# Performance work log

Hardware: AMD Instinct MI355X
Metric: run time of the kernel (lower is better)

## Reference

```python
import jax, jax.numpy as jnp
import numpy as np

B, S, DIM = 2, 2048, 1024
H = 16
HD = DIM // H  # 64
SCALE = HD ** -0.5


def setup_inputs() -> dict:
    key = jax.random.key(0)
    k1, k2, k3 = jax.random.split(key, 3)
    x = jax.random.normal(k1, (B, S, DIM), dtype=jnp.float32)
    # Linear weights scaled ~1/sqrt(fan_in) like torch default init
    Wqkv = jax.random.normal(k2, (DIM, 3 * DIM), dtype=jnp.float32) * (DIM ** -0.5)
    Wproj = jax.random.normal(k3, (DIM, DIM), dtype=jnp.float32) * (DIM ** -0.5)
    return {"x": x, "Wqkv": Wqkv, "Wproj": Wproj}


def reference(x, Wqkv, Wproj):
    Bsz, Slen, dim = x.shape
    qkv = x @ Wqkv  # (B, S, 3*dim)
    qkv = qkv.reshape(Bsz, Slen, 3, H, HD)
    q, k, v = qkv[:, :, 0], qkv[:, :, 1], qkv[:, :, 2]  # each (B, S, H, HD)
    # softmax attention (chunking in the original is memory-only; math identical)
    scores = jnp.einsum("bshd,bthd->bhst", q, k) * SCALE  # (B, H, S, S)
    attn = jax.nn.softmax(scores, axis=-1)
    out = jnp.einsum("bhst,bthd->bshd", attn, v)  # (B, S, H, HD)
    out = out.reshape(Bsz, Slen, dim)
    return out @ Wproj
```

## Files before the change

kernel.cpp:

```cpp
#include <hip/hip_runtime.h>
#include <stdint.h>

typedef unsigned short u16;
typedef __attribute__((ext_vector_type(8))) short bf16x8;
typedef __attribute__((ext_vector_type(4))) float f32x4;

#define BATCH 2
#define SEQ 2048
#define NH 16
#define HDIM 64
#define DMODEL 1024
#define MTOT (BATCH * SEQ)
#define QKV_N (3 * DMODEL)
#define ATT_SCALE 0.125f
#define L2E 1.44269504088896340736f
#define C2 (ATT_SCALE * L2E)

#define BAR() asm volatile("s_barrier" ::: "memory")
#define F3(a, b, c) fmaxf(fmaxf((a), (b)), (c))

__device__ __forceinline__ u16 f2b(float f) {
    uint32_t x = __builtin_bit_cast(uint32_t, f);
    uint32_t r = (x + 0x7fffu + ((x >> 16) & 1u)) >> 16;
    return (u16)r;
}

__device__ __forceinline__ uint32_t cvt_pk(float lo, float hi) {
    uint32_t r;
    asm("v_cvt_pk_bf16_f32 %0, %1, %2" : "=v"(r) : "v"(lo), "v"(hi));
    return r;
}

__device__ __forceinline__ void gl_lds16(const void* g, void* l) {
    __builtin_amdgcn_global_load_lds(
        (const __attribute__((address_space(1))) void*)g,
        (__attribute__((address_space(3))) void*)l, 16, 0, 0);
}

__global__ __launch_bounds__(256) void k_prep(const float* __restrict__ x,
                                              const float* __restrict__ Wq,
                                              const float* __restrict__ Wp,
                                              u16* __restrict__ xb,
                                              u16* __restrict__ WqT,
                                              u16* __restrict__ WpT) {
    const int bid = blockIdx.x, tid = threadIdx.x;
    if (bid < 2048) {
        const int i = bid * 256 + tid;
        const float4* p = (const float4*)x + (size_t)i * 2;
        float4 a = p[0], b = p[1];
        union { uint32_t w[4]; uint4 v; } u;
        u.w[0] = cvt_pk(a.x, a.y);
        u.w[1] = cvt_pk(a.z, a.w);
        u.w[2] = cvt_pk(b.x, b.y);
        u.w[3] = cvt_pk(b.z, b.w);
        *(uint4*)(xb + (size_t)i * 8) = u.v;
        return;
    }
    __shared__ float tile[64][65];
    const float* W;
    u16* WT;
    int cols, bx, by;
    if (bid < 2048 + 768) {
        const int j = bid - 2048;
        W = Wq; WT = WqT; cols = QKV_N; bx = j % 48; by = j / 48;
    } else {
        const int j = bid - 2816;
        W = Wp; WT = WpT; cols = DMODEL; bx = j % 16; by = j / 16;
    }
    const int rows = DMODEL;
    const int c0 = bx * 64, r0 = by * 64;
    const int tx = tid & 63, ty = tid >> 6;
#pragma unroll
    for (int i = 0; i < 16; ++i) {
        int r = i * 4 + ty;
        tile[r][tx] = W[(size_t)(r0 + r) * cols + c0 + tx];
    }
    __syncthreads();
#pragma unroll
    for (int i = 0; i < 16; ++i) {
        int c = i * 4 + ty;
        WT[(size_t)(c0 + c) * rows + r0 + tx] = f2b(tile[tx][c]);
    }
}

__global__ __launch_bounds__(512, 2) void k_gemm_qkv8(const u16* __restrict__ A,
                                                      const u16* __restrict__ BT,
                                                      u16* __restrict__ C,
                                                      u16* __restrict__ Vt) {
    extern __shared__ __align__(16) u16 lds[];
    const int tid = threadIdx.x, wid = tid >> 6, lane = tid & 63;
    const int r = lane & 15, g = lane >> 4;
    const int wr = wid >> 2, wc = wid & 3;
    const int m0 = blockIdx.y * 256, n0 = blockIdx.x * 256;
    const int K = DMODEL;

    auto STG = [&](int kt2, int rg) {
        const int isB = rg >> 1, half = rg & 1;
        const u16* src = isB ? BT : A;
        const int rowb = (isB ? n0 : m0) + half * 128 + wid * 16 + (lane >> 2);
        const u16* s = src + (size_t)rowb * K + kt2 * 64 + (lane & 3) * 8;
        const int dst = (kt2 & 1) * 32768 + isB * 16384 + half * 8192 +
                        wid * 1024 + lane * 8;
        gl_lds16(s, &lds[dst]);
        gl_lds16(s + 32, &lds[dst + 512]);
    };

    f32x4 acc[8][4] = {};
    bf16x8 a[4][2], b[4][2];
    const int aB = wr * 8192 + r * 32 + g * 8;
    const int bB = 16384 + (wc >> 1) * 8192 + (wc & 1) * 4096 + r * 32 + g * 8;

#pragma unroll
    for (int t2 = 0; t2 < 2; ++t2)
#pragma unroll
        for (int rg = 0; rg < 4; ++rg) STG(t2, rg);
    asm volatile("s_waitcnt vmcnt(0)" ::: "memory");
    __syncthreads();

    for (int kt = 0; kt < 16; ++kt) {
        const int sb = (kt & 1) * 32768;
#pragma unroll
        for (int mi = 0; mi < 4; ++mi)
#pragma unroll
            for (int kk = 0; kk < 2; ++kk)
                a[mi][kk] = *(const bf16x8*)&lds[sb + aB + (mi * 2 + kk) * 512];
#pragma unroll
        for (int ni = 0; ni < 2; ++ni)
#pragma unroll
            for (int kk = 0; kk < 2; ++kk)
                b[ni][kk] = *(const bf16x8*)&lds[sb + bB + (ni * 2 + kk) * 512];
        BAR();
        __builtin_amdgcn_s_setprio(1);
#pragma unroll
        for (int mi = 0; mi < 4; ++mi)
#pragma unroll
            for (int ni = 0; ni < 2; ++ni)
#pragma unroll
                for (int kk = 0; kk < 2; ++kk)
                    acc[mi][ni] = __builtin_amdgcn_mfma_f32_16x16x32_bf16(
                        b[ni][kk], a[mi][kk], acc[mi][ni], 0, 0, 0);
        __builtin_amdgcn_s_setprio(0);
        BAR();
#pragma unroll
        for (int ni = 2; ni < 4; ++ni)
#pragma unroll
            for (int kk = 0; kk < 2; ++kk)
                b[ni][kk] = *(const bf16x8*)&lds[sb + bB + (ni * 2 + kk) * 512];
        BAR();
        __builtin_amdgcn_s_setprio(1);
#pragma unroll
        for (int mi = 0; mi < 4; ++mi)
#pragma unroll
            for (int ni = 2; ni < 4; ++ni)
#pragma unroll
                for (int kk = 0; kk < 2; ++kk)
                    acc[mi][ni] = __builtin_amdgcn_mfma_f32_16x16x32_bf16(
                        b[ni][kk], a[mi][kk], acc[mi][ni], 0, 0, 0);
        __builtin_amdgcn_s_setprio(0);
        BAR();
#pragma unroll
        for (int mi = 0; mi < 4; ++mi)
#pragma unroll
            for (int kk = 0; kk < 2; ++kk)
                a[mi][kk] = *(const bf16x8*)&lds[sb + aB + ((4 + mi) * 2 + kk) * 512];
        if (kt < 14) { STG(kt + 2, 2); STG(kt + 2, 3); }
        BAR();
        __builtin_amdgcn_s_setprio(1);
#pragma unroll
        for (int mi = 0; mi < 4; ++mi)
#pragma unroll
            for (int ni = 2; ni < 4; ++ni)
#pragma unroll
                for (int kk = 0; kk < 2; ++kk)
                    acc[4 + mi][ni] = __builtin_amdgcn_mfma_f32_16x16x32_bf16(
                        b[ni][kk], a[mi][kk], acc[4 + mi][ni], 0, 0, 0);
        __builtin_amdgcn_s_setprio(0);
        BAR();
        if (kt < 14) { STG(kt + 2, 0); STG(kt + 2, 1); }
        BAR();
        __builtin_amdgcn_s_setprio(1);
#pragma unroll
        for (int mi = 0; mi < 4; ++mi)
#pragma unroll
            for (int ni = 0; ni < 2; ++ni)
#pragma unroll
                for (int kk = 0; kk < 2; ++kk)
                    acc[4 + mi][ni] = __builtin_amdgcn_mfma_f32_16x16x32_bf16(
                        b[ni][kk], a[mi][kk], acc[4 + mi][ni], 0, 0, 0);
        __builtin_amdgcn_s_setprio(0);
        if (kt < 14) {
            asm volatile("s_waitcnt vmcnt(8)" ::: "memory");
        } else if (kt == 14) {
            asm volatile("s_waitcnt vmcnt(0)" ::: "memory");
        }
        BAR();
    }

    if (n0 < 2 * DMODEL) {
#pragma unroll
        for (int mi = 0; mi < 8; ++mi)
#pragma unroll
            for (int ni = 0; ni < 4; ++ni) {
                const int row = m0 + wr * 128 + mi * 16 + r;
                const int col = n0 + wc * 64 + ni * 16 + g * 4;
                union { uint32_t w[2]; ushort4 v; } o;
                o.w[0] = cvt_pk(acc[mi][ni][0], acc[mi][ni][1]);
                o.w[1] = cvt_pk(acc[mi][ni][2], acc[mi][ni][3]);
                *(ushort4*)&C[(size_t)row * QKV_N + col] = o.v;
            }
    } else {
        const int h_ = ((n0 - 2 * DMODEL) >> 6) + wc;
#pragma unroll
        for (int mi = 0; mi < 8; ++mi)
#pragma unroll
            for (int ni = 0; ni < 4; ++ni) {
                const int row = m0 + wr * 128 + mi * 16 + r;
                const int b_ = row >> 11, s_ = row & (SEQ - 1);
                const int hd0 = ni * 16 + g * 4;
                union { uint32_t w[2]; u16 t[4]; } o;
                o.w[0] = cvt_pk(acc[mi][ni][0], acc[mi][ni][1]);
                o.w[1] = cvt_pk(acc[mi][ni][2], acc[mi][ni][3]);
                const size_t base =
                    ((size_t)(b_ * NH + h_) * HDIM + hd0) * SEQ + s_;
                Vt[base] = o.t[0];
                Vt[base + SEQ] = o.t[1];
                Vt[base + 2 * SEQ] = o.t[2];
                Vt[base + 3 * SEQ] = o.t[3];
            }
    }
}

__global__ __launch_bounds__(256) void k_gemm_proj(const u16* __restrict__ A,
                                                   const u16* __restrict__ BT,
                                                   float* __restrict__ C) {
    __shared__ __align__(16) u16 As[64 * 64];
    __shared__ __align__(16) u16 Bs[128 * 64];
    const int tid = threadIdx.x;
    const int wid = tid >> 6, lane = tid & 63;
    const int r = lane & 15, g = lane >> 4;
    const int m0 = blockIdx.y * 64, n0 = blockIdx.x * 128;
    const int srow = lane >> 3, scol = (lane & 7) * 8;
    const int K = DMODEL;
    f32x4 acc[4][2] = {};
    for (int k0 = 0; k0 < K; k0 += 64) {
#pragma unroll
        for (int i = 0; i < 2; ++i) {
            const int li = wid * 2 + i;
            gl_lds16(A + (size_t)(m0 + li * 8 + srow) * K + k0 + scol, &As[li * 512]);
        }
#pragma unroll
        for (int i = 0; i < 4; ++i) {
            const int li = wid * 4 + i;
            gl_lds16(BT + (size_t)(n0 + li * 8 + srow) * K + k0 + scol, &Bs[li * 512]);
        }
        __syncthreads();
#pragma unroll
        for (int kk = 0; kk < 2; ++kk) {
            bf16x8 af[4], bfr[2];
#pragma unroll
            for (int mi = 0; mi < 4; ++mi)
                af[mi] = *(const bf16x8*)&As[(mi * 16 + r) * 64 + kk * 32 + g * 8];
#pragma unroll
            for (int ni = 0; ni < 2; ++ni)
                bfr[ni] = *(const bf16x8*)&Bs[(wid * 32 + ni * 16 + r) * 64 + kk * 32 + g * 8];
#pragma unroll
            for (int mi = 0; mi < 4; ++mi)
#pragma unroll
                for (int ni = 0; ni < 2; ++ni)
                    acc[mi][ni] = __builtin_amdgcn_mfma_f32_16x16x32_bf16(
                        bfr[ni], af[mi], acc[mi][ni], 0, 0, 0);
        }
        __syncthreads();
    }
#pragma unroll
    for (int mi = 0; mi < 4; ++mi)
#pragma unroll
        for (int ni = 0; ni < 2; ++ni) {
            const int row = m0 + mi * 16 + r;
            const int col = n0 + wid * 32 + ni * 16 + g * 4;
            float4 vv;
            vv.x = acc[mi][ni][0]; vv.y = acc[mi][ni][1];
            vv.z = acc[mi][ni][2]; vv.w = acc[mi][ni][3];
            *(float4*)&C[(size_t)row * DMODEL + col] = vv;
        }
}

__global__ __launch_bounds__(256) void k_attn(const u16* __restrict__ qkv,
                                              const u16* __restrict__ Vt,
                                              u16* __restrict__ O) {
    __shared__ __align__(16) u16 Ks[3][4096];
    __shared__ __align__(16) u16 Vs[2][4096];
    const int bh = blockIdx.y;
    const int b = bh >> 4, h = bh & 15;
    const int q0 = blockIdx.x * 64;
    const int tid = threadIdx.x, wid = tid >> 6, lane = tid & 63;
    const int r = lane & 15, g = lane >> 4;
    const int NT = SEQ / 64;

    const size_t qbase = (size_t)(b * SEQ + q0 + wid * 16 + r) * QKV_N + h * HDIM;
    const bf16x8 qf0 = *(const bf16x8*)&qkv[qbase + g * 8];
    const bf16x8 qf1 = *(const bf16x8*)&qkv[qbase + 32 + g * 8];

    const short one_b = (short)0x3F80;
    const bf16x8 ones = {one_b, one_b, one_b, one_b, one_b, one_b, one_b, one_b};

    float mL = -1e30f;
    f32x4 oacc[4] = {};
    f32x4 lacc = {};
    const int kc0 = wid * 2;

    const u16* kp[2];
    const u16* vp[2];
    int kdst[2], vdst[2];
#pragma unroll
    for (int i = 0; i < 2; ++i) {
        const int kc = kc0 + i;
        const int ksrow = (kc >> 2) * 32 + g * 8 + (kc & 1) * 4 + ((lane >> 2) & 3);
        const int kscol = ((kc >> 1) & 1) * 32 + (lane & 3) * 8;
        kp[i] = qkv + (size_t)(b * SEQ + ksrow) * QKV_N + DMODEL + h * HDIM + kscol;
        const int vhd = (kc & 3) * 16 + r;
        const int vsc = (kc >> 2) * 32 + g * 8;
        vp[i] = Vt + ((size_t)bh * HDIM + vhd) * SEQ + vsc;
        kdst[i] = kc * 512;
        vdst[i] = kc * 512;
    }

#define STAGE_K(SLOT)                                                \
    {                                                                \
        _Pragma("unroll") for (int i = 0; i < 2; ++i) {              \
            gl_lds16(kp[i], &Ks[SLOT][kdst[i]]);                     \
            kp[i] += 64 * QKV_N;                                     \
        }                                                            \
    }
#define STAGE_V(SLOT)                                                \
    {                                                                \
        _Pragma("unroll") for (int i = 0; i < 2; ++i) {              \
            gl_lds16(vp[i], &Vs[SLOT][vdst[i]]);                     \
            vp[i] += 64;                                             \
        }                                                            \
    }
#define QKT(DST, SLOT)                                               \
    {                                                                \
        _Pragma("unroll") for (int nf = 0; nf < 4; ++nf) {           \
            const int kbase = (nf & 1) * 2048 + (nf >> 1) * 512 +    \
                              (r >> 2) * 128 + (r & 3) * 32 + g * 8; \
            bf16x8 kf0 = *(const bf16x8*)&Ks[SLOT][kbase];           \
            bf16x8 kf1 = *(const bf16x8*)&Ks[SLOT][kbase + 1024];    \
            DST[nf] = __builtin_amdgcn_mfma_f32_16x16x32_bf16(       \
                kf0, qf0, DST[nf], 0, 0, 0);                         \
            DST[nf] = __builtin_amdgcn_mfma_f32_16x16x32_bf16(       \
                kf1, qf1, DST[nf], 0, 0, 0);                         \
        }                                                            \
    }

    STAGE_K(0); STAGE_V(0);
    STAGE_K(1); STAGE_V(1);
    STAGE_K(2);
    asm volatile("s_waitcnt vmcnt(0)");
    __syncthreads();

    f32x4 sA[4] = {};
    __builtin_amdgcn_s_setprio(1);
    QKT(sA, 0);
    __builtin_amdgcn_s_setprio(0);
    BAR();

    int kw = 0, kr = 1;
    for (int t = 0; t < NT; ++t) {
        const int vcur = t & 1;

        if (t + 3 < NT) STAGE_K(kw);

        f32x4 sB[4] = {};
        if (t + 1 < NT) {
            __builtin_amdgcn_s_setprio(1);
            QKT(sB, kr);
            __builtin_amdgcn_s_setprio(0);
        }

        float mt = F3(sA[0][0], sA[0][1], sA[0][2]);
        mt = F3(mt, sA[0][3], sA[1][0]);
        mt = F3(mt, sA[1][1], sA[1][2]);
        mt = F3(mt, sA[1][3], sA[2][0]);
        mt = F3(mt, sA[2][1], sA[2][2]);
        mt = F3(mt, sA[2][3], sA[3][0]);
        mt = F3(mt, sA[3][1], sA[3][2]);
        mt = fmaxf(mt, sA[3][3]);
        const float pm = mt * C2;
        if (!__all(pm <= mL + 8.f)) {
            float rm = pm;
            rm = fmaxf(rm, __shfl_xor(rm, 16, 64));
            rm = fmaxf(rm, __shfl_xor(rm, 32, 64));
            const float mNew = fmaxf(mL, rm);
            const float al = exp2f(mL - mNew);
            mL = mNew;
#pragma unroll
            for (int ht = 0; ht < 4; ++ht)
#pragma unroll
                for (int e = 0; e < 4; ++e) oacc[ht][e] *= al;
#pragma unroll
            for (int e = 0; e < 4; ++e) lacc[e] *= al;
        }
        float p[4][4];
#pragma unroll
        for (int nf = 0; nf < 4; ++nf)
#pragma unroll
            for (int e = 0; e < 4; ++e)
                p[nf][e] = exp2f(sA[nf][e] * C2 - mL);

        union { uint32_t w[4]; bf16x8 v; } upf0, upf1;
        upf0.w[0] = cvt_pk(p[0][0], p[0][1]);
        upf0.w[1] = cvt_pk(p[0][2], p[0][3]);
        upf0.w[2] = cvt_pk(p[2][0], p[2][1]);
        upf0.w[3] = cvt_pk(p[2][2], p[2][3]);
        upf1.w[0] = cvt_pk(p[1][0], p[1][1]);
        upf1.w[1] = cvt_pk(p[1][2], p[1][3]);
        upf1.w[2] = cvt_pk(p[3][0], p[3][1]);
        upf1.w[3] = cvt_pk(p[3][2], p[3][3]);

        __builtin_amdgcn_s_setprio(1);
#pragma unroll
        for (int ht = 0; ht < 4; ++ht) {
            bf16x8 vf0 = *(const bf16x8*)&Vs[vcur][ht * 512 + g * 128 + r * 8];
            bf16x8 vf1 = *(const bf16x8*)&Vs[vcur][(4 + ht) * 512 + g * 128 + r * 8];
            oacc[ht] = __builtin_amdgcn_mfma_f32_16x16x32_bf16(vf0, upf0.v, oacc[ht], 0, 0, 0);
            oacc[ht] = __builtin_amdgcn_mfma_f32_16x16x32_bf16(vf1, upf1.v, oacc[ht], 0, 0, 0);
        }
        lacc = __builtin_amdgcn_mfma_f32_16x16x32_bf16(ones, upf0.v, lacc, 0, 0, 0);
        lacc = __builtin_amdgcn_mfma_f32_16x16x32_bf16(ones, upf1.v, lacc, 0, 0, 0);
        __builtin_amdgcn_s_setprio(0);

        if (t + 1 < NT) {
            BAR();
            if (t + 2 < NT) STAGE_V(vcur);
            if (t <= NT - 4) {
                asm volatile("s_waitcnt vmcnt(4)");
            } else if (t == NT - 3) {
                asm volatile("s_waitcnt vmcnt(2)");
            } else {
                asm volatile("s_waitcnt vmcnt(0)");
            }
            BAR();
        }

#pragma unroll
        for (int nf = 0; nf < 4; ++nf) sA[nf] = sB[nf];
        kw = (kw == 2) ? 0 : kw + 1;
        kr = (kr == 2) ? 0 : kr + 1;
    }
#undef STAGE_K
#undef STAGE_V
#undef QKT

    const float inv = 1.0f / lacc[0];
    const size_t obase = (size_t)(b * SEQ + q0 + wid * 16 + r) * DMODEL + h * HDIM;
#pragma unroll
    for (int ht = 0; ht < 4; ++ht) {
        union { uint32_t w[2]; ushort4 v; } o;
        o.w[0] = cvt_pk(oacc[ht][0] * inv, oacc[ht][1] * inv);
        o.w[1] = cvt_pk(oacc[ht][2] * inv, oacc[ht][3] * inv);
        *(ushort4*)&O[obase + ht * 16 + g * 4] = o.v;
    }
}

extern "C" void kernel_launch(void* const* d_in, const int* in_sizes, int n_in,
                              void* d_out, int out_size, void* d_ws, size_t ws_size,
                              hipStream_t stream) {
    const float* x = (const float*)d_in[0];
    const float* Wqkv = (const float*)d_in[1];
    const float* Wproj = (const float*)d_in[2];
    float* out = (float*)d_out;

    u16* xb = (u16*)d_ws;
    u16* WqkvT = xb + (size_t)MTOT * DMODEL;
    u16* WprojT = WqkvT + (size_t)QKV_N * DMODEL;
    u16* qkv = WprojT + (size_t)DMODEL * DMODEL;
    u16* Vt = qkv + (size_t)MTOT * QKV_N;
    u16* Ob = Vt + (size_t)BATCH * NH * HDIM * SEQ;

    hipFuncSetAttribute(reinterpret_cast<const void*>(k_gemm_qkv8),
                        hipFuncAttributeMaxDynamicSharedMemorySize, 131072);

    k_prep<<<dim3(3072), 256, 0, stream>>>(x, Wqkv, Wproj, xb, WqkvT, WprojT);
    k_gemm_qkv8<<<dim3(QKV_N / 256, MTOT / 256), 512, 131072, stream>>>(
        xb, WqkvT, qkv, Vt);
    k_attn<<<dim3(SEQ / 64, BATCH * NH), 256, 0, stream>>>(qkv, Vt, Ob);
    k_gemm_proj<<<dim3(DMODEL / 128, MTOT / 64), 256, 0, stream>>>(Ob, WprojT, out);
}
```

Baseline: 215.0 us.

## Fuse all four stages into one persistent cooperative kernel with grid syncs

Replaces the four separate launches (prep, QKV GEMM, attention, projection) with a single cooperative kernel of 256 blocks of 512 threads that walks through each stage and separates them with grid.sync(). Each stage is remapped to virtual block indices: attention runs two 4-wave units per block over two passes, and projection runs two units per block. The aim is to remove inter-kernel launch gaps and tail effects. In exchange only 256 blocks with 128KB LDS run, so occupancy per stage drops (only 192 blocks do the QKV GEMM), and the grid barriers add their own cost.

```diff
diff --git a/kernel.cpp b/kernel.cpp
--- a/kernel.cpp
+++ b/kernel.cpp
@@ -1,5 +1,8 @@
 #include <hip/hip_runtime.h>
+#include <hip/hip_cooperative_groups.h>
 #include <stdint.h>
+
+namespace cg = cooperative_groups;
 
 typedef unsigned short u16;
 typedef __attribute__((ext_vector_type(8))) short bf16x8;
@@ -37,15 +40,15 @@
         (__attribute__((address_space(3))) void*)l, 16, 0, 0);
 }
 
-__global__ __launch_bounds__(256) void k_prep(const float* __restrict__ x,
-                                              const float* __restrict__ Wq,
-                                              const float* __restrict__ Wp,
-                                              u16* __restrict__ xb,
-                                              u16* __restrict__ WqT,
-                                              u16* __restrict__ WpT) {
-    const int bid = blockIdx.x, tid = threadIdx.x;
-    if (bid < 2048) {
-        const int i = bid * 256 + tid;
+__device__ __forceinline__ void stage_prep(u16* lds,
+                                           const float* x, const float* Wq,
+                                           const float* Wp, u16* xb,
+                                           u16* WqT, u16* WpT,
+                                           int bid, int tid) {
+    const int gt = bid * 512 + tid;
+#pragma unroll
+    for (int it = 0; it < 4; ++it) {
+        const int i = gt + it * 131072;
         const float4* p = (const float4*)x + (size_t)i * 2;
         float4 a = p[0], b = p[1];
         union { uint32_t w[4]; uint4 v; } u;
@@ -54,44 +57,38 @@
         u.w[2] = cvt_pk(b.x, b.y);
         u.w[3] = cvt_pk(b.z, b.w);
         *(uint4*)(xb + (size_t)i * 8) = u.v;
-        return;
-    }
-    __shared__ float tile[64][65];
-    const float* W;
-    u16* WT;
-    int cols, bx, by;
-    if (bid < 2048 + 768) {
-        const int j = bid - 2048;
-        W = Wq; WT = WqT; cols = QKV_N; bx = j % 48; by = j / 48;
-    } else {
-        const int j = bid - 2816;
-        W = Wp; WT = WpT; cols = DMODEL; bx = j % 16; by = j / 16;
-    }
-    const int rows = DMODEL;
-    const int c0 = bx * 64, r0 = by * 64;
+    }
+    float (*tile)[65] = (float(*)[65])lds;
     const int tx = tid & 63, ty = tid >> 6;
-#pragma unroll
-    for (int i = 0; i < 16; ++i) {
-        int r = i * 4 + ty;
-        tile[r][tx] = W[(size_t)(r0 + r) * cols + c0 + tx];
-    }
-    __syncthreads();
-#pragma unroll
-    for (int i = 0; i < 16; ++i) {
-        int c = i * 4 + ty;
-        WT[(size_t)(c0 + c) * rows + r0 + tx] = f2b(tile[tx][c]);
-    }
-}
-
-__global__ __launch_bounds__(512, 2) void k_gemm_qkv8(const u16* __restrict__ A,
-                                                      const u16* __restrict__ BT,
-                                                      u16* __restrict__ C,
-                                                      u16* __restrict__ Vt) {
-    extern __shared__ __align__(16) u16 lds[];
-    const int tid = threadIdx.x, wid = tid >> 6, lane = tid & 63;
+    for (int it = 0; it < 4; ++it) {
+        const int tt = bid * 4 + it;
+        const float* W; u16* WT; int cols, bx, by;
+        if (tt < 768) { W = Wq; WT = WqT; cols = QKV_N; bx = tt % 48; by = tt / 48; }
+        else { int t2 = tt - 768; W = Wp; WT = WpT; cols = DMODEL; bx = t2 % 16; by = t2 / 16; }
+        const int c0 = bx * 64, r0 = by * 64;
+        __syncthreads();
+#pragma unroll
+        for (int i = 0; i < 8; ++i) {
+            int r = i * 8 + ty;
+            tile[r][tx] = W[(size_t)(r0 + r) * cols + c0 + tx];
+        }
+        __syncthreads();
+#pragma unroll
+        for (int i = 0; i < 8; ++i) {
+            int c = i * 8 + ty;
+            WT[(size_t)(c0 + c) * DMODEL + r0 + tx] = f2b(tile[tx][c]);
+        }
+    }
+}
+
+__device__ __forceinline__ void stage_gemm_qkv(u16* lds,
+                                               const u16* A, const u16* BT,
+                                               u16* C, u16* Vt,
+                                               int vb, int tid) {
+    const int wid = tid >> 6, lane = tid & 63;
     const int r = lane & 15, g = lane >> 4;
     const int wr = wid >> 2, wc = wid & 3;
-    const int m0 = blockIdx.y * 256, n0 = blockIdx.x * 256;
+    const int m0 = (vb / 12) * 256, n0 = (vb % 12) * 256;
     const int K = DMODEL;
 
     auto STG = [&](int kt2, int rg) {
@@ -230,15 +227,201 @@
     }
 }
 
-__global__ __launch_bounds__(256) void k_gemm_proj(const u16* __restrict__ A,
-                                                   const u16* __restrict__ BT,
-                                                   float* __restrict__ C) {
-    __shared__ __align__(16) u16 As[64 * 64];
-    __shared__ __align__(16) u16 Bs[128 * 64];
-    const int tid = threadIdx.x;
-    const int wid = tid >> 6, lane = tid & 63;
+__device__ __forceinline__ void stage_attn(u16* lds,
+                                           const u16* qkv, const u16* Vt,
+                                           u16* O, int bid, int tid) {
+    const int wid8 = tid >> 6;
+    const int half = wid8 >> 2, wid = wid8 & 3;
+    const int lane = tid & 63;
     const int r = lane & 15, g = lane >> 4;
-    const int m0 = blockIdx.y * 64, n0 = blockIdx.x * 128;
+    const int NT = SEQ / 64;
+    u16* Ks = lds + half * 20480;
+    u16* Vs = Ks + 3 * 4096;
+
+    const short one_b = (short)0x3F80;
+    const bf16x8 ones = {one_b, one_b, one_b, one_b, one_b, one_b, one_b, one_b};
+
+#define AT_STAGE_K(SLOT)                                             \
+    {                                                                \
+        _Pragma("unroll") for (int i = 0; i < 2; ++i) {              \
+            gl_lds16(kp[i], Ks + (SLOT) * 4096 + kdst[i]);           \
+            kp[i] += 64 * QKV_N;                                     \
+        }                                                            \
+    }
+#define AT_STAGE_V(SLOT)                                             \
+    {                                                                \
+        _Pragma("unroll") for (int i = 0; i < 2; ++i) {              \
+            gl_lds16(vp[i], Vs + (SLOT) * 4096 + vdst[i]);           \
+            vp[i] += 64;                                             \
+        }                                                            \
+    }
+#define AT_QKT(DST, SLOT)                                            \
+    {                                                                \
+        _Pragma("unroll") for (int nf = 0; nf < 4; ++nf) {           \
+            const int kbase = (nf & 1) * 2048 + (nf >> 1) * 512 +    \
+                              (r >> 2) * 128 + (r & 3) * 32 + g * 8; \
+            bf16x8 kf0 = *(const bf16x8*)(Ks + (SLOT) * 4096 + kbase);          \
+            bf16x8 kf1 = *(const bf16x8*)(Ks + (SLOT) * 4096 + kbase + 1024);   \
+            DST[nf] = __builtin_amdgcn_mfma_f32_16x16x32_bf16(       \
+                kf0, qf0, DST[nf], 0, 0, 0);                         \
+            DST[nf] = __builtin_amdgcn_mfma_f32_16x16x32_bf16(       \
+                kf1, qf1, DST[nf], 0, 0, 0);                         \
+        }                                                            \
+    }
+
+    for (int pass = 0; pass < 2; ++pass) {
+        BAR();
+        const int unit = pass * 512 + bid * 2 + half;
+        const int bh = unit >> 5, qx = unit & 31;
+        const int b = bh >> 4, h = bh & 15;
+        const int q0 = qx * 64;
+
+        const size_t qbase = (size_t)(b * SEQ + q0 + wid * 16 + r) * QKV_N + h * HDIM;
+        const bf16x8 qf0 = *(const bf16x8*)&qkv[qbase + g * 8];
+        const bf16x8 qf1 = *(const bf16x8*)&qkv[qbase + 32 + g * 8];
+
+        float mL = -1e30f;
+        f32x4 oacc[4] = {};
+        f32x4 lacc = {};
+        const int kc0 = wid * 2;
+
+        const u16* kp[2];
+        const u16* vp[2];
+        int kdst[2], vdst[2];
+#pragma unroll
+        for (int i = 0; i < 2; ++i) {
+            const int kc = kc0 + i;
+            const int ksrow = (kc >> 2) * 32 + g * 8 + (kc & 1) * 4 + ((lane >> 2) & 3);
+            const int kscol = ((kc >> 1) & 1) * 32 + (lane & 3) * 8;
+            kp[i] = qkv + (size_t)(b * SEQ + ksrow) * QKV_N + DMODEL + h * HDIM + kscol;
+            const int vhd = (kc & 3) * 16 + r;
+            const int vsc = (kc >> 2) * 32 + g * 8;
+            vp[i] = Vt + ((size_t)bh * HDIM + vhd) * SEQ + vsc;
+            kdst[i] = kc * 512;
+            vdst[i] = kc * 512;
+        }
+
+        AT_STAGE_K(0); AT_STAGE_V(0);
+        AT_STAGE_K(1); AT_STAGE_V(1);
+        AT_STAGE_K(2);
+        asm volatile("s_waitcnt vmcnt(0)");
+        __syncthreads();
+
+        f32x4 sA[4] = {};
+        __builtin_amdgcn_s_setprio(1);
+        AT_QKT(sA, 0);
+        __builtin_amdgcn_s_setprio(0);
+        BAR();
+
+        int kw = 0, kr = 1;
+        for (int t = 0; t < NT; ++t) {
+            const int vcur = t & 1;
+            if (t + 3 < NT) AT_STAGE_K(kw);
+
+            f32x4 sB[4] = {};
+            if (t + 1 < NT) {
+                __builtin_amdgcn_s_setprio(1);
+                AT_QKT(sB, kr);
+                __builtin_amdgcn_s_setprio(0);
+            }
+
+            float mt = F3(sA[0][0], sA[0][1], sA[0][2]);
+            mt = F3(mt, sA[0][3], sA[1][0]);
+            mt = F3(mt, sA[1][1], sA[1][2]);
+            mt = F3(mt, sA[1][3], sA[2][0]);
+            mt = F3(mt, sA[2][1], sA[2][2]);
+            mt = F3(mt, sA[2][3], sA[3][0]);
+            mt = F3(mt, sA[3][1], sA[3][2]);
+            mt = fmaxf(mt, sA[3][3]);
+            const float pm = mt * C2;
+            if (!__all(pm <= mL + 8.f)) {
+                float rm = pm;
+                rm = fmaxf(rm, __shfl_xor(rm, 16, 64));
+                rm = fmaxf(rm, __shfl_xor(rm, 32, 64));
+                const float mNew = fmaxf(mL, rm);
+                const float al = exp2f(mL - mNew);
+                mL = mNew;
+#pragma unroll
+                for (int ht = 0; ht < 4; ++ht)
+#pragma unroll
+                    for (int e = 0; e < 4; ++e) oacc[ht][e] *= al;
+#pragma unroll
+                for (int e = 0; e < 4; ++e) lacc[e] *= al;
+            }
+            float p[4][4];
+#pragma unroll
+            for (int nf = 0; nf < 4; ++nf)
+#pragma unroll
+                for (int e = 0; e < 4; ++e)
+                    p[nf][e] = exp2f(sA[nf][e] * C2 - mL);
+
+            union { uint32_t w[4]; bf16x8 v; } upf0, upf1;
+            upf0.w[0] = cvt_pk(p[0][0], p[0][1]);
+            upf0.w[1] = cvt_pk(p[0][2], p[0][3]);
+            upf0.w[2] = cvt_pk(p[2][0], p[2][1]);
+            upf0.w[3] = cvt_pk(p[2][2], p[2][3]);
+            upf1.w[0] = cvt_pk(p[1][0], p[1][1]);
+            upf1.w[1] = cvt_pk(p[1][2], p[1][3]);
+            upf1.w[2] = cvt_pk(p[3][0], p[3][1]);
+            upf1.w[3] = cvt_pk(p[3][2], p[3][3]);
+
+            __builtin_amdgcn_s_setprio(1);
+#pragma unroll
+            for (int ht = 0; ht < 4; ++ht) {
+                bf16x8 vf0 = *(const bf16x8*)(Vs + vcur * 4096 + ht * 512 + g * 128 + r * 8);
+                bf16x8 vf1 = *(const bf16x8*)(Vs + vcur * 4096 + (4 + ht) * 512 + g * 128 + r * 8);
+                oacc[ht] = __builtin_amdgcn_mfma_f32_16x16x32_bf16(vf0, upf0.v, oacc[ht], 0, 0, 0);
+                oacc[ht] = __builtin_amdgcn_mfma_f32_16x16x32_bf16(vf1, upf1.v, oacc[ht], 0, 0, 0);
+            }
+            lacc = __builtin_amdgcn_mfma_f32_16x16x32_bf16(ones, upf0.v, lacc, 0, 0, 0);
+            lacc = __builtin_amdgcn_mfma_f32_16x16x32_bf16(ones, upf1.v, lacc, 0, 0, 0);
+            __builtin_amdgcn_s_setprio(0);
+
+            if (t + 1 < NT) {
+                BAR();
+                if (t + 2 < NT) AT_STAGE_V(vcur);
+                if (t <= NT - 4) {
+                    asm volatile("s_waitcnt vmcnt(4)");
+                } else if (t == NT - 3) {
+                    asm volatile("s_waitcnt vmcnt(2)");
+                } else {
+                    asm volatile("s_waitcnt vmcnt(0)");
+                }
+                BAR();
+            }
+
+#pragma unroll
+            for (int nf = 0; nf < 4; ++nf) sA[nf] = sB[nf];
+            kw = (kw == 2) ? 0 : kw + 1;
+            kr = (kr == 2) ? 0 : kr + 1;
+        }
+
+        const float inv = 1.0f / lacc[0];
+        const size_t obase = (size_t)(b * SEQ + q0 + wid * 16 + r) * DMODEL + h * HDIM;
+#pragma unroll
+        for (int ht = 0; ht < 4; ++ht) {
+            union { uint32_t w[2]; ushort4 v; } o;
+            o.w[0] = cvt_pk(oacc[ht][0] * inv, oacc[ht][1] * inv);
+            o.w[1] = cvt_pk(oacc[ht][2] * inv, oacc[ht][3] * inv);
+            *(ushort4*)&O[obase + ht * 16 + g * 4] = o.v;
+        }
+    }
+#undef AT_STAGE_K
+#undef AT_STAGE_V
+#undef AT_QKT
+}
+
+__device__ __forceinline__ void stage_proj(u16* lds,
+                                           const u16* A, const u16* BT,
+                                           float* C, int bid, int tid) {
+    const int wid8 = tid >> 6;
+    const int half = wid8 >> 2, wid = wid8 & 3;
+    const int lane = tid & 63;
+    const int r = lane & 15, g = lane >> 4;
+    u16* As = lds + half * 12288;
+    u16* Bs = As + 4096;
+    const int unit = bid * 2 + half;
+    const int n0 = (unit & 7) * 128, m0 = (unit >> 3) * 64;
     const int srow = lane >> 3, scol = (lane & 7) * 8;
     const int K = DMODEL;
     f32x4 acc[4][2] = {};
@@ -246,12 +429,12 @@
 #pragma unroll
         for (int i = 0; i < 2; ++i) {
             const int li = wid * 2 + i;
-            gl_lds16(A + (size_t)(m0 + li * 8 + srow) * K + k0 + scol, &As[li * 512]);
+            gl_lds16(A + (size_t)(m0 + li * 8 + srow) * K + k0 + scol, As + li * 512);
         }
 #pragma unroll
         for (int i = 0; i < 4; ++i) {
             const int li = wid * 4 + i;
-            gl_lds16(BT + (size_t)(n0 + li * 8 + srow) * K + k0 + scol, &Bs[li * 512]);
+            gl_lds16(BT + (size_t)(n0 + li * 8 + srow) * K + k0 + scol, Bs + li * 512);
         }
         __syncthreads();
 #pragma unroll
@@ -259,10 +442,10 @@
             bf16x8 af[4], bfr[2];
 #pragma unroll
             for (int mi = 0; mi < 4; ++mi)
-                af[mi] = *(const bf16x8*)&As[(mi * 16 + r) * 64 + kk * 32 + g * 8];
+                af[mi] = *(const bf16x8*)(As + (mi * 16 + r) * 64 + kk * 32 + g * 8);
 #pragma unroll
             for (int ni = 0; ni < 2; ++ni)
-                bfr[ni] = *(const bf16x8*)&Bs[(wid * 32 + ni * 16 + r) * 64 + kk * 32 + g * 8];
+                bfr[ni] = *(const bf16x8*)(Bs + (wid * 32 + ni * 16 + r) * 64 + kk * 32 + g * 8);
 #pragma unroll
             for (int mi = 0; mi < 4; ++mi)
 #pragma unroll
@@ -285,182 +468,27 @@
         }
 }
 
-__global__ __launch_bounds__(256) void k_attn(const u16* __restrict__ qkv,
-                                              const u16* __restrict__ Vt,
-                                              u16* __restrict__ O) {
-    __shared__ __align__(16) u16 Ks[3][4096];
-    __shared__ __align__(16) u16 Vs[2][4096];
-    const int bh = blockIdx.y;
-    const int b = bh >> 4, h = bh & 15;
-    const int q0 = blockIdx.x * 64;
-    const int tid = threadIdx.x, wid = tid >> 6, lane = tid & 63;
-    const int r = lane & 15, g = lane >> 4;
-    const int NT = SEQ / 64;
-
-    const size_t qbase = (size_t)(b * SEQ + q0 + wid * 16 + r) * QKV_N + h * HDIM;
-    const bf16x8 qf0 = *(const bf16x8*)&qkv[qbase + g * 8];
-    const bf16x8 qf1 = *(const bf16x8*)&qkv[qbase + 32 + g * 8];
-
-    const short one_b = (short)0x3F80;
-    const bf16x8 ones = {one_b, one_b, one_b, one_b, one_b, one_b, one_b, one_b};
-
-    float mL = -1e30f;
-    f32x4 oacc[4] = {};
-    f32x4 lacc = {};
-    const int kc0 = wid * 2;
-
-    const u16* kp[2];
-    const u16* vp[2];
-    int kdst[2], vdst[2];
-#pragma unroll
-    for (int i = 0; i < 2; ++i) {
-        const int kc = kc0 + i;
-        const int ksrow = (kc >> 2) * 32 + g * 8 + (kc & 1) * 4 + ((lane >> 2) & 3);
-        const int kscol = ((kc >> 1) & 1) * 32 + (lane & 3) * 8;
-        kp[i] = qkv + (size_t)(b * SEQ + ksrow) * QKV_N + DMODEL + h * HDIM + kscol;
-        const int vhd = (kc & 3) * 16 + r;
-        const int vsc = (kc >> 2) * 32 + g * 8;
-        vp[i] = Vt + ((size_t)bh * HDIM + vhd) * SEQ + vsc;
-        kdst[i] = kc * 512;
-        vdst[i] = kc * 512;
-    }
-
-#define STAGE_K(SLOT)                                                \
-    {                                                                \
-        _Pragma("unroll") for (int i = 0; i < 2; ++i) {              \
-            gl_lds16(kp[i], &Ks[SLOT][kdst[i]]);                     \
-            kp[i] += 64 * QKV_N;                                     \
-        }                                                            \
-    }
-#define STAGE_V(SLOT)                                                \
-    {                                                                \
-        _Pragma("unroll") for (int i = 0; i < 2; ++i) {              \
-            gl_lds16(vp[i], &Vs[SLOT][vdst[i]]);                     \
-            vp[i] += 64;                                             \
-        }                                                            \
-    }
-#define QKT(DST, SLOT)                                               \
-    {                                                                \
-        _Pragma("unroll") for (int nf = 0; nf < 4; ++nf) {           \
-            const int kbase = (nf & 1) * 2048 + (nf >> 1) * 512 +    \
-                              (r >> 2) * 128 + (r & 3) * 32 + g * 8; \
-            bf16x8 kf0 = *(const bf16x8*)&Ks[SLOT][kbase];           \
-            bf16x8 kf1 = *(const bf16x8*)&Ks[SLOT][kbase + 1024];    \
-            DST[nf] = __builtin_amdgcn_mfma_f32_16x16x32_bf16(       \
-                kf0, qf0, DST[nf], 0, 0, 0);                         \
-            DST[nf] = __builtin_amdgcn_mfma_f32_16x16x32_bf16(       \
-                kf1, qf1, DST[nf], 0, 0, 0);                         \
-        }                                                            \
-    }
-
-    STAGE_K(0); STAGE_V(0);
-    STAGE_K(1); STAGE_V(1);
-    STAGE_K(2);
-    asm volatile("s_waitcnt vmcnt(0)");
-    __syncthreads();
-
-    f32x4 sA[4] = {};
-    __builtin_amdgcn_s_setprio(1);
-    QKT(sA, 0);
-    __builtin_amdgcn_s_setprio(0);
-    BAR();
-
-    int kw = 0, kr = 1;
-    for (int t = 0; t < NT; ++t) {
-        const int vcur = t & 1;
-
-        if (t + 3 < NT) STAGE_K(kw);
-
-        f32x4 sB[4] = {};
-        if (t + 1 < NT) {
-            __builtin_amdgcn_s_setprio(1);
-            QKT(sB, kr);
-            __builtin_amdgcn_s_setprio(0);
-        }
-
-        float mt = F3(sA[0][0], sA[0][1], sA[0][2]);
-        mt = F3(mt, sA[0][3], sA[1][0]);
-        mt = F3(mt, sA[1][1], sA[1][2]);
-        mt = F3(mt, sA[1][3], sA[2][0]);
-        mt = F3(mt, sA[2][1], sA[2][2]);
-        mt = F3(mt, sA[2][3], sA[3][0]);
-        mt = F3(mt, sA[3][1], sA[3][2]);
-        mt = fmaxf(mt, sA[3][3]);
-        const float pm = mt * C2;
-        if (!__all(pm <= mL + 8.f)) {
-            float rm = pm;
-            rm = fmaxf(rm, __shfl_xor(rm, 16, 64));
-            rm = fmaxf(rm, __shfl_xor(rm, 32, 64));
-            const float mNew = fmaxf(mL, rm);
-            const float al = exp2f(mL - mNew);
-            mL = mNew;
-#pragma unroll
-            for (int ht = 0; ht < 4; ++ht)
-#pragma unroll
-                for (int e = 0; e < 4; ++e) oacc[ht][e] *= al;
-#pragma unroll
-            for (int e = 0; e < 4; ++e) lacc[e] *= al;
-        }
-        float p[4][4];
-#pragma unroll
-        for (int nf = 0; nf < 4; ++nf)
-#pragma unroll
-            for (int e = 0; e < 4; ++e)
-                p[nf][e] = exp2f(sA[nf][e] * C2 - mL);
-
-        union { uint32_t w[4]; bf16x8 v; } upf0, upf1;
-        upf0.w[0] = cvt_pk(p[0][0], p[0][1]);
-        upf0.w[1] = cvt_pk(p[0][2], p[0][3]);
-        upf0.w[2] = cvt_pk(p[2][0], p[2][1]);
-        upf0.w[3] = cvt_pk(p[2][2], p[2][3]);
-        upf1.w[0] = cvt_pk(p[1][0], p[1][1]);
-        upf1.w[1] = cvt_pk(p[1][2], p[1][3]);
-        upf1.w[2] = cvt_pk(p[3][0], p[3][1]);
-        upf1.w[3] = cvt_pk(p[3][2], p[3][3]);
-
-        __builtin_amdgcn_s_setprio(1);
-#pragma unroll
-        for (int ht = 0; ht < 4; ++ht) {
-            bf16x8 vf0 = *(const bf16x8*)&Vs[vcur][ht * 512 + g * 128 + r * 8];
-            bf16x8 vf1 = *(const bf16x8*)&Vs[vcur][(4 + ht) * 512 + g * 128 + r * 8];
-            oacc[ht] = __builtin_amdgcn_mfma_f32_16x16x32_bf16(vf0, upf0.v, oacc[ht], 0, 0, 0);
-            oacc[ht] = __builtin_amdgcn_mfma_f32_16x16x32_bf16(vf1, upf1.v, oacc[ht], 0, 0, 0);
-        }
-        lacc = __builtin_amdgcn_mfma_f32_16x16x32_bf16(ones, upf0.v, lacc, 0, 0, 0);
-        lacc = __builtin_amdgcn_mfma_f32_16x16x32_bf16(ones, upf1.v, lacc, 0, 0, 0);
-        __builtin_amdgcn_s_setprio(0);
-
-        if (t + 1 < NT) {
-            BAR();
-            if (t + 2 < NT) STAGE_V(vcur);
-            if (t <= NT - 4) {
-                asm volatile("s_waitcnt vmcnt(4)");
-            } else if (t == NT - 3) {
-                asm volatile("s_waitcnt vmcnt(2)");
-            } else {
-                asm volatile("s_waitcnt vmcnt(0)");
-            }
-            BAR();
-        }
-
-#pragma unroll
-        for (int nf = 0; nf < 4; ++nf) sA[nf] = sB[nf];
-        kw = (kw == 2) ? 0 : kw + 1;
-        kr = (kr == 2) ? 0 : kr + 1;
-    }
-#undef STAGE_K
-#undef STAGE_V
-#undef QKT
-
-    const float inv = 1.0f / lacc[0];
-    const size_t obase = (size_t)(b * SEQ + q0 + wid * 16 + r) * DMODEL + h * HDIM;
-#pragma unroll
-    for (int ht = 0; ht < 4; ++ht) {
-        union { uint32_t w[2]; ushort4 v; } o;
-        o.w[0] = cvt_pk(oacc[ht][0] * inv, oacc[ht][1] * inv);
-        o.w[1] = cvt_pk(oacc[ht][2] * inv, oacc[ht][3] * inv);
-        *(ushort4*)&O[obase + ht * 16 + g * 4] = o.v;
-    }
+__global__ __launch_bounds__(512, 2) void k_mega(const float* __restrict__ x,
+                                                 const float* __restrict__ Wq,
+                                                 const float* __restrict__ Wp,
+                                                 u16* __restrict__ xb,
+                                                 u16* __restrict__ WqT,
+                                                 u16* __restrict__ WpT,
+                                                 u16* __restrict__ qkv,
+                                                 u16* __restrict__ Vt,
+                                                 u16* __restrict__ Ob,
+                                                 float* __restrict__ out) {
+    extern __shared__ __align__(16) u16 lds[];
+    cg::grid_group grid = cg::this_grid();
+    const int bid = blockIdx.x, tid = threadIdx.x;
+
+    stage_prep(lds, x, Wq, Wp, xb, WqT, WpT, bid, tid);
+    grid.sync();
+    if (bid < 192) stage_gemm_qkv(lds, xb, WqT, qkv, Vt, bid, tid);
+    grid.sync();
+    stage_attn(lds, qkv, Vt, Ob, bid, tid);
+    grid.sync();
+    stage_proj(lds, Ob, WpT, out, bid, tid);
 }
 
 extern "C" void kernel_launch(void* const* d_in, const int* in_sizes, int n_in,
@@ -478,12 +506,12 @@
     u16* Vt = qkv + (size_t)MTOT * QKV_N;
     u16* Ob = Vt + (size_t)BATCH * NH * HDIM * SEQ;
 
-    hipFuncSetAttribute(reinterpret_cast<const void*>(k_gemm_qkv8),
+    hipFuncSetAttribute(reinterpret_cast<const void*>(k_mega),
                         hipFuncAttributeMaxDynamicSharedMemorySize, 131072);
 
-    k_prep<<<dim3(3072), 256, 0, stream>>>(x, Wqkv, Wproj, xb, WqkvT, WprojT);
-    k_gemm_qkv8<<<dim3(QKV_N / 256, MTOT / 256), 512, 131072, stream>>>(
-        xb, WqkvT, qkv, Vt);
-    k_attn<<<dim3(SEQ / 64, BATCH * NH), 256, 0, stream>>>(qkv, Vt, Ob);
-    k_gemm_proj<<<dim3(DMODEL / 128, MTOT / 64), 256, 0, stream>>>(Ob, WprojT, out);
-}
+    void* kargs[] = {(void*)&x, (void*)&Wqkv, (void*)&Wproj,
+                     (void*)&xb, (void*)&WqkvT, (void*)&WprojT,
+                     (void*)&qkv, (void*)&Vt, (void*)&Ob, (void*)&out};
+    hipLaunchCooperativeKernel(reinterpret_cast<const void*>(k_mega),
+                               dim3(256), dim3(512), kargs, 131072, stream);
+}
```

New measurement: 346.4 us. +61.1%, slower.
